# Optimization experiments

Measured on AMD Instinct MI355X. Metric: run time of the kernel, lower is better.

Reference implementation:

```python
import jax, jax.numpy as jnp
import numpy as np

CHANNELS = 64
K = 3
STRIDE = 1
GROUP_CHANNELS = 2
GROUPS = CHANNELS // GROUP_CHANNELS  # 32
RED = 4
PAD = (K - 1) // 2


def setup_inputs() -> dict:
    key = jax.random.key(0)
    ks = jax.random.split(key, 6)
    x = jax.random.normal(ks[0], (8, CHANNELS, 128, 128), dtype=jnp.float32)
    w1 = jax.random.normal(ks[1], (CHANNELS // RED, CHANNELS), dtype=jnp.float32) * 0.05
    b1 = jax.random.normal(ks[2], (CHANNELS // RED,), dtype=jnp.float32) * 0.05
    prelu_a = jnp.full((1,), 0.25, dtype=jnp.float32)
    w2 = jax.random.normal(ks[3], (K * K * GROUPS, CHANNELS // RED), dtype=jnp.float32) * 0.05
    b2 = jax.random.normal(ks[4], (K * K * GROUPS,), dtype=jnp.float32) * 0.05
    return {"x": x, "w1": w1, "b1": b1, "prelu_a": prelu_a, "w2": w2, "b2": b2}


def reference(x, w1, b1, prelu_a, w2, b2):
    # stride == 1: no avgpool
    # 1x1 conv -> PReLU -> 1x1 conv to generate per-pixel kernels
    t = jnp.einsum('bchw,oc->bohw', x, w1) + b1[None, :, None, None]
    t = jnp.where(t >= 0, t, prelu_a[0] * t)  # PReLU, single shared slope
    weight = jnp.einsum('bchw,oc->bohw', t, w2) + b2[None, :, None, None]
    b, _, h, w = weight.shape
    # (b, groups, 1, k^2, h, w)
    weight = weight.reshape(b, GROUPS, 1, K * K, h, w)
    # unfold: im2col with padding 1, stride 1; channel-major (c, kh, kw) ordering like torch.nn.Unfold
    xp = jnp.pad(x, ((0, 0), (0, 0), (PAD, PAD), (PAD, PAD)))
    patches = jnp.stack(
        [xp[:, :, i:i + h, j:j + w] for i in range(K) for j in range(K)], axis=2
    )  # (b, c, k^2, h, w)
    patches = patches.reshape(b, GROUPS, GROUP_CHANNELS, K * K, h, w)
    out = (weight * patches).sum(axis=3).reshape(b, CHANNELS, h, w)
    return out
```

## Files before the change

### kernel.cpp

```cpp
#include <hip/hip_runtime.h>

#define NPIX (128 * 128)
#define CH 64
#define RMID 16
#define KK 9
#define PLANE_B 65536

typedef float v2f __attribute__((ext_vector_type(2)));

#define ASM_LOAD2(dst, voff) \
    asm volatile("global_load_dwordx2 %0, %1, %2" \
                 : "=v"(dst) : "v"((uint32_t)(voff)), "s"(xbc))

#define VMWAIT(N) do { \
    asm volatile("s_waitcnt vmcnt(" #N ")" ::: "memory"); \
    __builtin_amdgcn_sched_barrier(0); \
} while (0)

#define ISSUE8(B, oct) do { \
    const uint32_t c0 = (uint32_t)pb0 + (uint32_t)((oct) * 8) * 65536u; \
    ASM_LOAD2(B##0, c0); \
    ASM_LOAD2(B##1, c0 + 1u * 65536u); \
    ASM_LOAD2(B##2, c0 + 2u * 65536u); \
    ASM_LOAD2(B##3, c0 + 3u * 65536u); \
    ASM_LOAD2(B##4, c0 + 4u * 65536u); \
    ASM_LOAD2(B##5, c0 + 5u * 65536u); \
    ASM_LOAD2(B##6, c0 + 6u * 65536u); \
    ASM_LOAD2(B##7, c0 + 7u * 65536u); \
} while (0)

#define FMA8(xvreg, ch) do { \
    _Pragma("unroll") \
    for (int r = 0; r < RMID; ++r) { \
        const float w = w1[r * CH + (ch)]; \
        v2f wv; wv.x = w; wv.y = w; \
        t2[r] = __builtin_elementwise_fma(wv, (xvreg), t2[r]); \
    } \
} while (0)

#define CONSUME8(B, oct) do { \
    FMA8(B##0, (oct) * 8 + 0); \
    FMA8(B##1, (oct) * 8 + 1); \
    FMA8(B##2, (oct) * 8 + 2); \
    FMA8(B##3, (oct) * 8 + 3); \
    FMA8(B##4, (oct) * 8 + 4); \
    FMA8(B##5, (oct) * 8 + 5); \
    FMA8(B##6, (oct) * 8 + 6); \
    FMA8(B##7, (oct) * 8 + 7); \
} while (0)

#define ISSUE_TAPS(B, gg) do { \
    const uint32_t q0 = (uint32_t)pb0 + (uint32_t)(2 * (gg)) * 65536u; \
    const uint32_t q1 = q0 + 65536u; \
    ASM_LOAD2(B##A0, q0 + (uint32_t)ro0); \
    ASM_LOAD2(B##A1, q0); \
    ASM_LOAD2(B##A2, q0 + (uint32_t)ro2); \
    ASM_LOAD2(B##E0, q1 + (uint32_t)ro0); \
    ASM_LOAD2(B##E1, q1); \
    ASM_LOAD2(B##E2, q1 + (uint32_t)ro2); \
} while (0)

__device__ __forceinline__ void group_tail(
    int g, v2f tA0, v2f tA1, v2f tA2, v2f tE0, v2f tE1, v2f tE2,
    float mL, float mR, v2f rm0v, v2f rm2v,
    const v2f (&t2)[RMID], const float* __restrict__ w2,
    const float* __restrict__ b2, char* obc, int pb0)
{
    const v2f A0 = tA0 * rm0v;
    const v2f A1 = tA1;
    const v2f A2 = tA2 * rm2v;
    const v2f E0 = tE0 * rm0v;
    const v2f E1 = tE1;
    const v2f E2 = tE2 * rm2v;

    const float lA0 = __shfl_up(A0.y, 1), rA0 = __shfl_down(A0.x, 1);
    const float lA1 = __shfl_up(A1.y, 1), rA1 = __shfl_down(A1.x, 1);
    const float lA2 = __shfl_up(A2.y, 1), rA2 = __shfl_down(A2.x, 1);
    const float lE0 = __shfl_up(E0.y, 1), rE0 = __shfl_down(E0.x, 1);
    const float lE1 = __shfl_up(E1.y, 1), rE1 = __shfl_down(E1.x, 1);
    const float lE2 = __shfl_up(E2.y, 1), rE2 = __shfl_down(E2.x, 1);

    v2f oA; oA.x = 0.f; oA.y = 0.f;
    v2f oB = oA;
#pragma unroll
    for (int k = 0; k < KK; ++k) {
        const float* w2r = w2 + (g * KK + k) * RMID;
        const float bb = b2[g * KK + k];
        v2f acc; acc.x = bb; acc.y = bb;
#pragma unroll
        for (int r = 0; r < RMID; ++r) {
            const float w = w2r[r];
            v2f wv; wv.x = w; wv.y = w;
            acc = __builtin_elementwise_fma(wv, t2[r], acc);
        }
        if (k == 0 || k == 3 || k == 6) acc.x *= mL;
        if (k == 2 || k == 5 || k == 8) acc.y *= mR;

        const v2f Ar = (k < 3) ? A0 : (k < 6) ? A1 : A2;
        const v2f Er = (k < 3) ? E0 : (k < 6) ? E1 : E2;
        const float lA = (k < 3) ? lA0 : (k < 6) ? lA1 : lA2;
        const float rA = (k < 3) ? rA0 : (k < 6) ? rA1 : rA2;
        const float lE = (k < 3) ? lE0 : (k < 6) ? lE1 : lE2;
        const float rE = (k < 3) ? rE0 : (k < 6) ? rE1 : rE2;

        v2f tpA, tpE;
        if (k % 3 == 0)      { tpA.x = lA;   tpA.y = Ar.x;
                               tpE.x = lE;   tpE.y = Er.x; }
        else if (k % 3 == 1) { tpA = Ar;     tpE = Er;     }
        else                 { tpA.x = Ar.y; tpA.y = rA;
                               tpE.x = Er.y; tpE.y = rE;   }
        oA = __builtin_elementwise_fma(acc, tpA, oA);
        oB = __builtin_elementwise_fma(acc, tpE, oB);
    }

    __builtin_nontemporal_store(oA, (v2f*)(obc + (size_t)(2 * g)     * PLANE_B + pb0));
    __builtin_nontemporal_store(oB, (v2f*)(obc + (size_t)(2 * g + 1) * PLANE_B + pb0));
}

__global__ __launch_bounds__(256, 2) void invol_fused(
    const float* __restrict__ x,
    const float* __restrict__ w1,
    const float* __restrict__ b1,
    const float* __restrict__ prelu_a,
    const float* __restrict__ w2,
    const float* __restrict__ b2,
    float* __restrict__ out)
{
    const int c    = threadIdx.x & 63;
    const int rsub = threadIdx.x >> 6;

    const int L     = blockIdx.x;
    const int bq    = L & 7;
    const int go    = (L >> 3) & 3;
    const int strip = L >> 5;

    const int hq  = 4 * strip + rsub;
    const int p0  = hq * 128 + 2 * c;
    const int pb0 = 4 * p0;

    const float* xb  = x + (size_t)bq * CH * NPIX;
    const char*  xbc = (const char*)xb;

    const float rm0 = (hq > 0)   ? 1.f : 0.f;
    const float rm2 = (hq < 127) ? 1.f : 0.f;
    const float mL  = (c > 0)    ? 1.f : 0.f;
    const float mR  = (c < 63)   ? 1.f : 0.f;
    const int   ro0 = (hq > 0)   ? -512 : 0;
    const int   ro2 = (hq < 127) ?  512 : 0;

    v2f xA0, xA1, xA2, xA3, xA4, xA5, xA6, xA7;
    v2f xB0, xB1, xB2, xB3, xB4, xB5, xB6, xB7;
    v2f taA0, taA1, taA2, taE0, taE1, taE2;
    v2f tbA0, tbA1, tbA2, tbE0, tbE1, tbE2;

    ISSUE_TAPS(ta, 8 * go + 0);
    ISSUE8(xA, 0);
    ISSUE8(xB, 1);

    v2f t2[RMID];
#pragma unroll
    for (int r = 0; r < RMID; ++r) {
        const float b = b1[r];
        t2[r].x = b; t2[r].y = b;
    }

    VMWAIT(8);  CONSUME8(xA, 0); ISSUE8(xA, 2);
    VMWAIT(8);  CONSUME8(xB, 1); ISSUE8(xB, 3);
    VMWAIT(8);  CONSUME8(xA, 2); ISSUE8(xA, 4);
    VMWAIT(8);  CONSUME8(xB, 3); ISSUE8(xB, 5);
    VMWAIT(8);  CONSUME8(xA, 4); ISSUE8(xA, 6);
    VMWAIT(8);  CONSUME8(xB, 5); ISSUE8(xB, 7);
    VMWAIT(8);  CONSUME8(xA, 6);
    VMWAIT(0);  CONSUME8(xB, 7);

    {
        const float a = prelu_a[0];
        v2f av; av.x = a; av.y = a;
        v2f z;  z.x = 0.f; z.y = 0.f;
#pragma unroll
        for (int r = 0; r < RMID; ++r) {
            const v2f pos = __builtin_elementwise_max(t2[r], z);
            const v2f neg = __builtin_elementwise_min(t2[r], z);
            t2[r] = __builtin_elementwise_fma(av, neg, pos);
        }
    }

    v2f rm0v; rm0v.x = rm0; rm0v.y = rm0;
    v2f rm2v; rm2v.x = rm2; rm2v.y = rm2;

    char* obc = (char*)(out + (size_t)bq * CH * NPIX);
    const int g0 = 8 * go;

    ISSUE_TAPS(tb, g0 + 1); VMWAIT(6);
    group_tail(g0 + 0, taA0, taA1, taA2, taE0, taE1, taE2, mL, mR, rm0v, rm2v, t2, w2, b2, obc, pb0);
    ISSUE_TAPS(ta, g0 + 2); VMWAIT(6);
    group_tail(g0 + 1, tbA0, tbA1, tbA2, tbE0, tbE1, tbE2, mL, mR, rm0v, rm2v, t2, w2, b2, obc, pb0);
    ISSUE_TAPS(tb, g0 + 3); VMWAIT(6);
    group_tail(g0 + 2, taA0, taA1, taA2, taE0, taE1, taE2, mL, mR, rm0v, rm2v, t2, w2, b2, obc, pb0);
    ISSUE_TAPS(ta, g0 + 4); VMWAIT(6);
    group_tail(g0 + 3, tbA0, tbA1, tbA2, tbE0, tbE1, tbE2, mL, mR, rm0v, rm2v, t2, w2, b2, obc, pb0);
    ISSUE_TAPS(tb, g0 + 5); VMWAIT(6);
    group_tail(g0 + 4, taA0, taA1, taA2, taE0, taE1, taE2, mL, mR, rm0v, rm2v, t2, w2, b2, obc, pb0);
    ISSUE_TAPS(ta, g0 + 6); VMWAIT(6);
    group_tail(g0 + 5, tbA0, tbA1, tbA2, tbE0, tbE1, tbE2, mL, mR, rm0v, rm2v, t2, w2, b2, obc, pb0);
    ISSUE_TAPS(tb, g0 + 7); VMWAIT(6);
    group_tail(g0 + 6, taA0, taA1, taA2, taE0, taE1, taE2, mL, mR, rm0v, rm2v, t2, w2, b2, obc, pb0);
    VMWAIT(2);
    group_tail(g0 + 7, tbA0, tbA1, tbA2, tbE0, tbE1, tbE2, mL, mR, rm0v, rm2v, t2, w2, b2, obc, pb0);
}

extern "C" void kernel_launch(void* const* d_in, const int* in_sizes, int n_in,
                              void* d_out, int out_size, void* d_ws, size_t ws_size,
                              hipStream_t stream)
{
    const float* x  = (const float*)d_in[0];
    const float* w1 = (const float*)d_in[1];
    const float* b1 = (const float*)d_in[2];
    const float* pa = (const float*)d_in[3];
    const float* w2 = (const float*)d_in[4];
    const float* b2 = (const float*)d_in[5];
    float* out = (float*)d_out;

    hipLaunchKernelGGL(invol_fused, dim3(1024), dim3(256), 0, stream,
                       x, w1, b1, pa, w2, b2, out);
}
```

Before: 112.5 us.

## Split fused kernel to compute reduction conv once per pixel via workspace

The fused kernel recomputed the 64->16 conv and PReLU in each of four channel-group blocks per pixel strip, which reads all 64 input channels four times. This splits the work into a conv1 kernel (256 blocks) that writes the 16-channel PReLU output to a workspace, and an apply kernel that reads it back along with the taps. This removes redundant x reads and FMAs, at the cost of a second launch, a workspace write/read round trip, and a serialization point between the kernels. The fused path is kept as a fallback when no workspace is provided.

```diff
diff --git a/kernel.cpp b/kernel.cpp
--- a/kernel.cpp
+++ b/kernel.cpp
@@ -5,28 +5,29 @@
 #define RMID 16
 #define KK 9
 #define PLANE_B 65536
+#define WS_NEEDED ((size_t)8 * RMID * NPIX * 4)
 
 typedef float v2f __attribute__((ext_vector_type(2)));
 
-#define ASM_LOAD2(dst, voff) \
+#define ASM_LOAD2(dst, base, voff) \
     asm volatile("global_load_dwordx2 %0, %1, %2" \
-                 : "=v"(dst) : "v"((uint32_t)(voff)), "s"(xbc))
+                 : "=v"(dst) : "v"((uint32_t)(voff)), "s"(base))
 
 #define VMWAIT(N) do { \
     asm volatile("s_waitcnt vmcnt(" #N ")" ::: "memory"); \
     __builtin_amdgcn_sched_barrier(0); \
 } while (0)
 
-#define ISSUE8(B, oct) do { \
+#define ISSUE8(B, base, oct) do { \
     const uint32_t c0 = (uint32_t)pb0 + (uint32_t)((oct) * 8) * 65536u; \
-    ASM_LOAD2(B##0, c0); \
-    ASM_LOAD2(B##1, c0 + 1u * 65536u); \
-    ASM_LOAD2(B##2, c0 + 2u * 65536u); \
-    ASM_LOAD2(B##3, c0 + 3u * 65536u); \
-    ASM_LOAD2(B##4, c0 + 4u * 65536u); \
-    ASM_LOAD2(B##5, c0 + 5u * 65536u); \
-    ASM_LOAD2(B##6, c0 + 6u * 65536u); \
-    ASM_LOAD2(B##7, c0 + 7u * 65536u); \
+    ASM_LOAD2(B##0, base, c0); \
+    ASM_LOAD2(B##1, base, c0 + 1u * 65536u); \
+    ASM_LOAD2(B##2, base, c0 + 2u * 65536u); \
+    ASM_LOAD2(B##3, base, c0 + 3u * 65536u); \
+    ASM_LOAD2(B##4, base, c0 + 4u * 65536u); \
+    ASM_LOAD2(B##5, base, c0 + 5u * 65536u); \
+    ASM_LOAD2(B##6, base, c0 + 6u * 65536u); \
+    ASM_LOAD2(B##7, base, c0 + 7u * 65536u); \
 } while (0)
 
 #define FMA8(xvreg, ch) do { \
@@ -52,12 +53,35 @@
 #define ISSUE_TAPS(B, gg) do { \
     const uint32_t q0 = (uint32_t)pb0 + (uint32_t)(2 * (gg)) * 65536u; \
     const uint32_t q1 = q0 + 65536u; \
-    ASM_LOAD2(B##A0, q0 + (uint32_t)ro0); \
-    ASM_LOAD2(B##A1, q0); \
-    ASM_LOAD2(B##A2, q0 + (uint32_t)ro2); \
-    ASM_LOAD2(B##E0, q1 + (uint32_t)ro0); \
-    ASM_LOAD2(B##E1, q1); \
-    ASM_LOAD2(B##E2, q1 + (uint32_t)ro2); \
+    ASM_LOAD2(B##A0, xbc, q0 + (uint32_t)ro0); \
+    ASM_LOAD2(B##A1, xbc, q0); \
+    ASM_LOAD2(B##A2, xbc, q0 + (uint32_t)ro2); \
+    ASM_LOAD2(B##E0, xbc, q1 + (uint32_t)ro0); \
+    ASM_LOAD2(B##E1, xbc, q1); \
+    ASM_LOAD2(B##E2, xbc, q1 + (uint32_t)ro2); \
+} while (0)
+
+#define PRELU_T2() do { \
+    const float a = prelu_a[0]; \
+    v2f av; av.x = a; av.y = a; \
+    v2f z;  z.x = 0.f; z.y = 0.f; \
+    _Pragma("unroll") \
+    for (int r = 0; r < RMID; ++r) { \
+        const v2f pos = __builtin_elementwise_max(t2[r], z); \
+        const v2f neg = __builtin_elementwise_min(t2[r], z); \
+        t2[r] = __builtin_elementwise_fma(av, neg, pos); \
+    } \
+} while (0)
+
+#define CONV1_LADDER() do { \
+    VMWAIT(8);  CONSUME8(xA, 0); ISSUE8(xA, xbc, 2); \
+    VMWAIT(8);  CONSUME8(xB, 1); ISSUE8(xB, xbc, 3); \
+    VMWAIT(8);  CONSUME8(xA, 2); ISSUE8(xA, xbc, 4); \
+    VMWAIT(8);  CONSUME8(xB, 3); ISSUE8(xB, xbc, 5); \
+    VMWAIT(8);  CONSUME8(xA, 4); ISSUE8(xA, xbc, 6); \
+    VMWAIT(8);  CONSUME8(xB, 5); ISSUE8(xB, xbc, 7); \
+    VMWAIT(8);  CONSUME8(xA, 6); \
+    VMWAIT(0);  CONSUME8(xB, 7); \
 } while (0)
 
 __device__ __forceinline__ void group_tail(
@@ -117,18 +141,56 @@
     __builtin_nontemporal_store(oB, (v2f*)(obc + (size_t)(2 * g + 1) * PLANE_B + pb0));
 }
 
-__global__ __launch_bounds__(256, 2) void invol_fused(
+__global__ __launch_bounds__(256, 2) void invol_conv1(
     const float* __restrict__ x,
     const float* __restrict__ w1,
     const float* __restrict__ b1,
     const float* __restrict__ prelu_a,
+    float* __restrict__ tws)
+{
+    const int c    = threadIdx.x & 63;
+    const int rsub = threadIdx.x >> 6;
+    const int L     = blockIdx.x;
+    const int bq    = L & 7;
+    const int strip = L >> 3;
+
+    const int hq  = 4 * strip + rsub;
+    const int p0  = hq * 128 + 2 * c;
+    const int pb0 = 4 * p0;
+
+    const char* xbc = (const char*)(x + (size_t)bq * CH * NPIX);
+
+    v2f xA0, xA1, xA2, xA3, xA4, xA5, xA6, xA7;
+    v2f xB0, xB1, xB2, xB3, xB4, xB5, xB6, xB7;
+
+    ISSUE8(xA, xbc, 0);
+    ISSUE8(xB, xbc, 1);
+
+    v2f t2[RMID];
+#pragma unroll
+    for (int r = 0; r < RMID; ++r) {
+        const float b = b1[r];
+        t2[r].x = b; t2[r].y = b;
+    }
+
+    CONV1_LADDER();
+    PRELU_T2();
+
+    char* twb = (char*)tws + (size_t)bq * RMID * PLANE_B;
+#pragma unroll
+    for (int r = 0; r < RMID; ++r)
+        *(v2f*)(twb + (size_t)r * PLANE_B + pb0) = t2[r];
+}
+
+__global__ __launch_bounds__(256, 2) void invol_apply(
+    const float* __restrict__ x,
     const float* __restrict__ w2,
     const float* __restrict__ b2,
+    const float* __restrict__ tws,
     float* __restrict__ out)
 {
     const int c    = threadIdx.x & 63;
     const int rsub = threadIdx.x >> 6;
-
     const int L     = blockIdx.x;
     const int bq    = L & 7;
     const int go    = (L >> 3) & 3;
@@ -138,8 +200,8 @@
     const int p0  = hq * 128 + 2 * c;
     const int pb0 = 4 * p0;
 
-    const float* xb  = x + (size_t)bq * CH * NPIX;
-    const char*  xbc = (const char*)xb;
+    const char* xbc = (const char*)(x + (size_t)bq * CH * NPIX);
+    const char* twc = (const char*)tws + (size_t)bq * RMID * PLANE_B;
 
     const float rm0 = (hq > 0)   ? 1.f : 0.f;
     const float rm2 = (hq < 127) ? 1.f : 0.f;
@@ -148,48 +210,20 @@
     const int   ro0 = (hq > 0)   ? -512 : 0;
     const int   ro2 = (hq < 127) ?  512 : 0;
 
-    v2f xA0, xA1, xA2, xA3, xA4, xA5, xA6, xA7;
-    v2f xB0, xB1, xB2, xB3, xB4, xB5, xB6, xB7;
+    v2f t2[RMID];
     v2f taA0, taA1, taA2, taE0, taE1, taE2;
     v2f tbA0, tbA1, tbA2, tbE0, tbE1, tbE2;
 
-    ISSUE_TAPS(ta, 8 * go + 0);
-    ISSUE8(xA, 0);
-    ISSUE8(xB, 1);
-
-    v2f t2[RMID];
-#pragma unroll
-    for (int r = 0; r < RMID; ++r) {
-        const float b = b1[r];
-        t2[r].x = b; t2[r].y = b;
-    }
-
-    VMWAIT(8);  CONSUME8(xA, 0); ISSUE8(xA, 2);
-    VMWAIT(8);  CONSUME8(xB, 1); ISSUE8(xB, 3);
-    VMWAIT(8);  CONSUME8(xA, 2); ISSUE8(xA, 4);
-    VMWAIT(8);  CONSUME8(xB, 3); ISSUE8(xB, 5);
-    VMWAIT(8);  CONSUME8(xA, 4); ISSUE8(xA, 6);
-    VMWAIT(8);  CONSUME8(xB, 5); ISSUE8(xB, 7);
-    VMWAIT(8);  CONSUME8(xA, 6);
-    VMWAIT(0);  CONSUME8(xB, 7);
-
-    {
-        const float a = prelu_a[0];
-        v2f av; av.x = a; av.y = a;
-        v2f z;  z.x = 0.f; z.y = 0.f;
-#pragma unroll
-        for (int r = 0; r < RMID; ++r) {
-            const v2f pos = __builtin_elementwise_max(t2[r], z);
-            const v2f neg = __builtin_elementwise_min(t2[r], z);
-            t2[r] = __builtin_elementwise_fma(av, neg, pos);
-        }
-    }
+#pragma unroll
+    for (int r = 0; r < RMID; ++r)
+        ASM_LOAD2(t2[r], twc, (uint32_t)pb0 + (uint32_t)r * 65536u);
+    const int g0 = 8 * go;
+    ISSUE_TAPS(ta, g0 + 0);
+    VMWAIT(6);
 
     v2f rm0v; rm0v.x = rm0; rm0v.y = rm0;
     v2f rm2v; rm2v.x = rm2; rm2v.y = rm2;
-
     char* obc = (char*)(out + (size_t)bq * CH * NPIX);
-    const int g0 = 8 * go;
 
     ISSUE_TAPS(tb, g0 + 1); VMWAIT(6);
     group_tail(g0 + 0, taA0, taA1, taA2, taE0, taE1, taE2, mL, mR, rm0v, rm2v, t2, w2, b2, obc, pb0);
@@ -209,6 +243,77 @@
     group_tail(g0 + 7, tbA0, tbA1, tbA2, tbE0, tbE1, tbE2, mL, mR, rm0v, rm2v, t2, w2, b2, obc, pb0);
 }
 
+__global__ __launch_bounds__(256, 2) void invol_fused(
+    const float* __restrict__ x,
+    const float* __restrict__ w1,
+    const float* __restrict__ b1,
+    const float* __restrict__ prelu_a,
+    const float* __restrict__ w2,
+    const float* __restrict__ b2,
+    float* __restrict__ out)
+{
+    const int c    = threadIdx.x & 63;
+    const int rsub = threadIdx.x >> 6;
+    const int L     = blockIdx.x;
+    const int bq    = L & 7;
+    const int go    = (L >> 3) & 3;
+    const int strip = L >> 5;
+
+    const int hq  = 4 * strip + rsub;
+    const int p0  = hq * 128 + 2 * c;
+    const int pb0 = 4 * p0;
+
+    const char* xbc = (const char*)(x + (size_t)bq * CH * NPIX);
+
+    const float rm0 = (hq > 0)   ? 1.f : 0.f;
+    const float rm2 = (hq < 127) ? 1.f : 0.f;
+    const float mL  = (c > 0)    ? 1.f : 0.f;
+    const float mR  = (c < 63)   ? 1.f : 0.f;
+    const int   ro0 = (hq > 0)   ? -512 : 0;
+    const int   ro2 = (hq < 127) ?  512 : 0;
+
+    v2f xA0, xA1, xA2, xA3, xA4, xA5, xA6, xA7;
+    v2f xB0, xB1, xB2, xB3, xB4, xB5, xB6, xB7;
+    v2f taA0, taA1, taA2, taE0, taE1, taE2;
+    v2f tbA0, tbA1, tbA2, tbE0, tbE1, tbE2;
+
+    const int g0 = 8 * go;
+    ISSUE_TAPS(ta, g0 + 0);
+    ISSUE8(xA, xbc, 0);
+    ISSUE8(xB, xbc, 1);
+
+    v2f t2[RMID];
+#pragma unroll
+    for (int r = 0; r < RMID; ++r) {
+        const float b = b1[r];
+        t2[r].x = b; t2[r].y = b;
+    }
+
+    CONV1_LADDER();
+    PRELU_T2();
+
+    v2f rm0v; rm0v.x = rm0; rm0v.y = rm0;
+    v2f rm2v; rm2v.x = rm2; rm2v.y = rm2;
+    char* obc = (char*)(out + (size_t)bq * CH * NPIX);
+
+    ISSUE_TAPS(tb, g0 + 1); VMWAIT(6);
+    group_tail(g0 + 0, taA0, taA1, taA2, taE0, taE1, taE2, mL, mR, rm0v, rm2v, t2, w2, b2, obc, pb0);
+    ISSUE_TAPS(ta, g0 + 2); VMWAIT(6);
+    group_tail(g0 + 1, tbA0, tbA1, tbA2, tbE0, tbE1, tbE2, mL, mR, rm0v, rm2v, t2, w2, b2, obc, pb0);
+    ISSUE_TAPS(tb, g0 + 3); VMWAIT(6);
+    group_tail(g0 + 2, taA0, taA1, taA2, taE0, taE1, taE2, mL, mR, rm0v, rm2v, t2, w2, b2, obc, pb0);
+    ISSUE_TAPS(ta, g0 + 4); VMWAIT(6);
+    group_tail(g0 + 3, tbA0, tbA1, tbA2, tbE0, tbE1, tbE2, mL, mR, rm0v, rm2v, t2, w2, b2, obc, pb0);
+    ISSUE_TAPS(tb, g0 + 5); VMWAIT(6);
+    group_tail(g0 + 4, taA0, taA1, taA2, taE0, taE1, taE2, mL, mR, rm0v, rm2v, t2, w2, b2, obc, pb0);
+    ISSUE_TAPS(ta, g0 + 6); VMWAIT(6);
+    group_tail(g0 + 5, tbA0, tbA1, tbA2, tbE0, tbE1, tbE2, mL, mR, rm0v, rm2v, t2, w2, b2, obc, pb0);
+    ISSUE_TAPS(tb, g0 + 7); VMWAIT(6);
+    group_tail(g0 + 6, taA0, taA1, taA2, taE0, taE1, taE2, mL, mR, rm0v, rm2v, t2, w2, b2, obc, pb0);
+    VMWAIT(2);
+    group_tail(g0 + 7, tbA0, tbA1, tbA2, tbE0, tbE1, tbE2, mL, mR, rm0v, rm2v, t2, w2, b2, obc, pb0);
+}
+
 extern "C" void kernel_launch(void* const* d_in, const int* in_sizes, int n_in,
                               void* d_out, int out_size, void* d_ws, size_t ws_size,
                               hipStream_t stream)
@@ -221,6 +326,14 @@
     const float* b2 = (const float*)d_in[5];
     float* out = (float*)d_out;
 
-    hipLaunchKernelGGL(invol_fused, dim3(1024), dim3(256), 0, stream,
-                       x, w1, b1, pa, w2, b2, out);
-}
+    if (d_ws != nullptr && ws_size >= WS_NEEDED) {
+        float* tws = (float*)d_ws;
+        hipLaunchKernelGGL(invol_conv1, dim3(256),  dim3(256), 0, stream,
+                           x, w1, b1, pa, tws);
+        hipLaunchKernelGGL(invol_apply, dim3(1024), dim3(256), 0, stream,
+                           x, w2, b2, tws, out);
+    } else {
+        hipLaunchKernelGGL(invol_fused, dim3(1024), dim3(256), 0, stream,
+                           x, w1, b1, pa, w2, b2, out);
+    }
+}
```

New measurement: 117.3 us. 4.3% more time.
